# Performance work log

Measured on AMD Instinct MI355X. Metric: run time of the kernel, lower is better.

Reference implementation:

```python
import jax, jax.numpy as jnp
import numpy as np

D_MODEL = 1024
NUM_HEADS = 16
D_HEAD = D_MODEL // NUM_HEADS
NEG_BIG = 10000000000.0  # matches the torch module's -1e10 mask constant


def setup_inputs() -> dict:
    key = jax.random.key(0)
    ks = jax.random.split(key, 9)
    d = D_MODEL
    scale = 1.0 / np.sqrt(d)
    inp = {
        "x": jax.random.normal(ks[0], (2, 2048, d), dtype=jnp.float32),
        "W_q": jax.random.normal(ks[1], (d, d), dtype=jnp.float32) * scale,
        "b_q": jnp.zeros((d,), dtype=jnp.float32),
        "W_k": jax.random.normal(ks[2], (d, d), dtype=jnp.float32) * scale,
        "b_k": jnp.zeros((d,), dtype=jnp.float32),
        "W_v": jax.random.normal(ks[3], (d, d), dtype=jnp.float32) * scale,
        "b_v": jnp.zeros((d,), dtype=jnp.float32),
        "W_o": jax.random.normal(ks[4], (d, d), dtype=jnp.float32) * scale,
        "b_o": jnp.zeros((d,), dtype=jnp.float32),
    }
    return inp


def reference(x, W_q, b_q, W_k, b_k, W_v, b_v, W_o, b_o):
    B, S, d = x.shape
    H, Dh = NUM_HEADS, D_HEAD

    Q = x @ W_q + b_q  # [B,S,d]
    K = x @ W_k + b_k
    V = x @ W_v + b_v

    # split heads: [B,S,d] -> [B,H,S,Dh]
    Qh = Q.reshape(B, S, H, Dh).transpose(0, 2, 1, 3)
    Kh = K.reshape(B, S, H, Dh).transpose(0, 2, 1, 3)
    Vh = V.reshape(B, S, H, Dh).transpose(0, 2, 1, 3)

    scores = jnp.einsum("bhid,bhjd->bhij", Qh, Kh) / jnp.sqrt(
        jnp.asarray(Dh, dtype=x.dtype)
    )

    # causal mask: tril(scores) - 1e10 * (1 - tril_mask)
    causal = jnp.tril(jnp.ones((S, S), dtype=x.dtype))
    scores = scores * causal - NEG_BIG * (1.0 - causal)

    attn = jax.nn.softmax(scores, axis=-1)  # dropout p=0.0 -> identity

    vals = jnp.einsum("bhij,bhjd->bhid", attn, Vh)  # [B,H,S,Dh]
    vals = vals.transpose(0, 2, 1, 3).reshape(B, S, d)

    return vals @ W_o + b_o
```

## Files before the change

### kernel.cpp

```cpp
#include <hip/hip_runtime.h>

typedef unsigned short u16;
typedef __attribute__((ext_vector_type(8))) short short8;
typedef __attribute__((ext_vector_type(4))) short shortx4;
typedef __attribute__((ext_vector_type(4))) float floatx4;

#define S_ 2048
#define D_ 1024
#define DQKV_ 3072
#define H_ 16
#define DH_ 64

#define EXP2F(x) __builtin_amdgcn_exp2f(x)

template <bool B> struct BoolC { static constexpr bool value = B; };

__device__ __forceinline__ float bf2f(u16 x) {
    union { unsigned int u; float f; } v; v.u = ((unsigned int)x) << 16; return v.f;
}
__device__ __forceinline__ u16 f2bf(float f) {
    unsigned int u = __float_as_uint(f);
    return (u16)((u + 0x7fffu + ((u >> 16) & 1u)) >> 16);
}
__device__ __forceinline__ unsigned int cvtpk_bf16(float lo, float hi) {
    unsigned int r;
    asm("v_cvt_pk_bf16_f32 %0, %1, %2" : "=v"(r) : "v"(lo), "v"(hi));
    return r;
}

__device__ __forceinline__ void async16(const void* g, void* l) {
    __builtin_amdgcn_global_load_lds(
        (const __attribute__((address_space(1))) unsigned int*)g,
        (__attribute__((address_space(3))) unsigned int*)l, 16, 0, 0);
}

__global__ __launch_bounds__(256) void convert_x(const float* __restrict__ x, u16* __restrict__ xb) {
    const size_t i = ((size_t)blockIdx.x * 256 + threadIdx.x) * 4;
    float4 v = *(const float4*)&x[i];
    shortx4 h;
    h[0] = (short)f2bf(v.x); h[1] = (short)f2bf(v.y);
    h[2] = (short)f2bf(v.z); h[3] = (short)f2bf(v.w);
    *(shortx4*)&xb[i] = h;
}

__global__ __launch_bounds__(256) void transpose_w4(const float* __restrict__ Wq, const float* __restrict__ Wk,
                                                    const float* __restrict__ Wv, const float* __restrict__ Wo,
                                                    u16* __restrict__ Wqkvt, u16* __restrict__ Wot) {
    __shared__ u16 tile[32][33];
    const int z = blockIdx.z;
    const float* W = (z == 0) ? Wq : (z == 1) ? Wk : (z == 2) ? Wv : Wo;
    u16* dst = (z == 3) ? Wot : (Wqkvt + (size_t)z * D_ * D_);
    const int tx = threadIdx.x, ty = threadIdx.y;
    const int n0 = blockIdx.x * 32, k0 = blockIdx.y * 32;
#pragma unroll
    for (int r = 0; r < 4; ++r) {
        int k = ty + r * 8;
        tile[k][tx] = f2bf(W[(size_t)(k0 + k) * D_ + n0 + tx]);
    }
    __syncthreads();
#pragma unroll
    for (int r = 0; r < 4; ++r) {
        int n = ty + r * 8;
        dst[(size_t)(n0 + n) * D_ + k0 + tx] = tile[tx][n];
    }
}

__global__ __launch_bounds__(256) void transpose_headV(const u16* __restrict__ QKV, u16* __restrict__ Vt) {
    __shared__ u16 tile[64 * 65];
    const int t = threadIdx.x;
    const int bh = blockIdx.y, b = bh >> 4, h = bh & 15;
    const int s0 = blockIdx.x << 6;
#pragma unroll
    for (int i = 0; i < 16; ++i) {
        int idx = t + (i << 8);
        int s = idx >> 6, d = idx & 63;
        tile[s * 65 + d] = QKV[(size_t)(b * S_ + s0 + s) * DQKV_ + 2048 + h * DH_ + d];
    }
    __syncthreads();
#pragma unroll
    for (int i = 0; i < 16; ++i) {
        int idx = t + (i << 8);
        int d = idx >> 6, p = idx & 63;
        int sk = ((p >> 5) << 5) | (((p >> 2) & 1) << 4) | (((p >> 3) & 3) << 2) | (p & 3);
        Vt[((size_t)bh * DH_ + d) * S_ + s0 + p] = tile[sk * 65 + d];
    }
}

template <int BM, int BN, bool OUTF32>
__global__ __launch_bounds__(256) void gemm_bt(const u16* __restrict__ A, const u16* __restrict__ Bt,
                                               const float* __restrict__ b0, const float* __restrict__ b1,
                                               const float* __restrict__ b2, void* __restrict__ Cp,
                                               int M, int N, int Kd) {
    constexpr int FI = BM / 32, FJ = BN / 32;
    __shared__ __align__(16) u16 As[2][BM * 32];
    __shared__ __align__(16) u16 Bs[2][BN * 32];
    const int t = threadIdx.x;
    const int m0 = blockIdx.y * BM, n0 = blockIdx.x * BN;
    const int w = t >> 6, lane = t & 63;
    const int lr = lane & 15, lg = lane >> 4;
    const int wm = (w >> 1) * (BM / 2), wn = (w & 1) * (BN / 2);
    const int srow = lane >> 2, scol = (lane & 3) << 3;
    floatx4 acc[FI][FJ] = {};

    auto stage = [&](int buf, int k0) {
#pragma unroll
        for (int c = 0; c < BM / 64; ++c) {
            int rbase = (w * (BM / 64) + c) * 16;
            async16(&A[(size_t)(m0 + rbase + srow) * Kd + k0 + scol], &As[buf][rbase * 32]);
        }
#pragma unroll
        for (int c = 0; c < BN / 64; ++c) {
            int rbase = (w * (BN / 64) + c) * 16;
            async16(&Bt[(size_t)(n0 + rbase + srow) * Kd + k0 + scol], &Bs[buf][rbase * 32]);
        }
    };

    stage(0, 0);
    const int nk = Kd / 32;
    for (int kk = 0; kk < nk; ++kk) {
        const int cur = kk & 1;
        __syncthreads();
        if (kk + 1 < nk) stage(cur ^ 1, (kk + 1) * 32);

        short8 af[FI], bfr[FJ];
#pragma unroll
        for (int i = 0; i < FI; ++i) af[i]  = *(const short8*)&As[cur][(wm + i * 16 + lr) * 32 + lg * 8];
#pragma unroll
        for (int j = 0; j < FJ; ++j) bfr[j] = *(const short8*)&Bs[cur][(wn + j * 16 + lr) * 32 + lg * 8];
#pragma unroll
        for (int i = 0; i < FI; ++i)
#pragma unroll
            for (int j = 0; j < FJ; ++j)
                acc[i][j] = __builtin_amdgcn_mfma_f32_16x16x32_bf16(af[i], bfr[j], acc[i][j], 0, 0, 0);
    }

#pragma unroll
    for (int j = 0; j < FJ; ++j) {
        int col = n0 + wn + j * 16 + lr;
        const float* bp = (col < 1024) ? b0 : (col < 2048) ? b1 : b2;
        float bv = bp[col & 1023];
#pragma unroll
        for (int i = 0; i < FI; ++i) {
            int rb = m0 + wm + i * 16 + lg * 4;
#pragma unroll
            for (int ii = 0; ii < 4; ++ii) {
                float val = acc[i][j][ii] + bv;
                if (OUTF32) ((float*)Cp)[(size_t)(rb + ii) * N + col] = val;
                else        ((u16*)Cp)[(size_t)(rb + ii) * N + col] = f2bf(val);
            }
        }
    }
}

__global__ __launch_bounds__(256) void attn_mfma(const u16* __restrict__ QKV, const u16* __restrict__ Vt,
                                                 u16* __restrict__ O) {
    __shared__ __align__(16) u16 KsA[2][64 * 64];
    __shared__ __align__(16) u16 VsA[2][64 * 64];
    const int t = threadIdx.x, w = t >> 6, lane = t & 63;
    const int lr = lane & 15, lg = lane >> 4;
    const int bh = blockIdx.x, b = bh >> 4, h = bh & 15;
    const int qt = 31 - blockIdx.y;
    const int q0 = qt << 6;
    const float cs = 0.18033688f;

    const u16* Kb  = QKV + (size_t)b * S_ * DQKV_ + 1024 + h * DH_;
    const u16* Vtb = Vt + (size_t)bh * DH_ * S_;

    const int rb = lane >> 3;
    const int cc = ((lane & 7) ^ rb) << 3;
    const int swz = lr & 7;

    short8 qf[2];
#pragma unroll
    for (int ks = 0; ks < 2; ++ks)
        qf[ks] = *(const short8*)&QKV[(size_t)(b * S_ + q0 + w * 16 + lr) * DQKV_ + h * DH_ + ks * 32 + lg * 8];

    floatx4 of[4] = {};
    float lsum = 0.f;

    auto stage = [&](int buf, int kbase) {
        u16* Kd = &KsA[buf][w * 512];
        u16* Vd = &VsA[buf][w * 512];
        async16(&Kb[(size_t)(kbase + w * 8 + rb) * DQKV_ + cc], Kd);
        async16(&Kb[(size_t)(kbase + 32 + w * 8 + rb) * DQKV_ + cc], Kd + 2048);
        async16(&Vtb[(size_t)(w * 8 + rb) * S_ + kbase + cc], Vd);
        async16(&Vtb[(size_t)(32 + w * 8 + rb) * S_ + kbase + cc], Vd + 2048);
    };

    stage(0, 0);

    auto body = [&](int kb, auto diagc) {
        constexpr bool DIAG = decltype(diagc)::value;
        const int cur = kb & 1;
        __syncthreads();
        if (kb < qt) stage(cur ^ 1, (kb + 1) << 6);
        const u16* Kc = KsA[cur];
        const u16* Vc = VsA[cur];

        floatx4 sf[4] = {};
#pragma unroll
        for (int ks = 0; ks < 2; ++ks)
#pragma unroll
            for (int tt = 0; tt < 4; ++tt) {
                short8 kf = *(const short8*)&Kc[(tt * 16 + lr) * 64 + ((((ks << 2) + lg) ^ swz) << 3)];
                sf[tt] = __builtin_amdgcn_mfma_f32_16x16x32_bf16(kf, qf[ks], sf[tt], 0, 0, 0);
            }

        float ev[4][4];
#pragma unroll
        for (int tt = 0; tt < 4; ++tt) {
            float s0;
#pragma unroll
            for (int ii = 0; ii < 4; ++ii) {
                float e = EXP2F(sf[tt][ii] * cs);
                if (DIAG && (tt * 16 + lg * 4 + ii > w * 16 + lr)) e = 0.f;
                ev[tt][ii] = e;
                s0 = (ii == 0) ? e : s0 + e;
            }
            lsum += s0;
        }

#pragma unroll
        for (int ks = 0; ks < 2; ++ks) {
            union { short8 s; unsigned int u[4]; } pk;
            pk.u[0] = cvtpk_bf16(ev[2 * ks][0], ev[2 * ks][1]);
            pk.u[1] = cvtpk_bf16(ev[2 * ks][2], ev[2 * ks][3]);
            pk.u[2] = cvtpk_bf16(ev[2 * ks + 1][0], ev[2 * ks + 1][1]);
            pk.u[3] = cvtpk_bf16(ev[2 * ks + 1][2], ev[2 * ks + 1][3]);
#pragma unroll
            for (int tt = 0; tt < 4; ++tt) {
                short8 vf = *(const short8*)&Vc[(tt * 16 + lr) * 64 + ((((ks << 2) + lg) ^ swz) << 3)];
                of[tt] = __builtin_amdgcn_mfma_f32_16x16x32_bf16(pk.s, vf, of[tt], 0, 0, 0);
            }
        }
    };

    for (int kb = 0; kb < qt; ++kb) body(kb, BoolC<false>{});
    body(qt, BoolC<true>{});

    lsum += __shfl_xor(lsum, 16);
    lsum += __shfl_xor(lsum, 32);
    const float rinv = 1.f / lsum;
    float rv[4];
#pragma unroll
    for (int ii = 0; ii < 4; ++ii)
        rv[ii] = __shfl(rinv, (lane & 48) | (lg * 4 + ii));

#pragma unroll
    for (int tt = 0; tt < 4; ++tt)
#pragma unroll
        for (int ii = 0; ii < 4; ++ii)
            O[(size_t)(b * S_ + q0 + w * 16 + lg * 4 + ii) * D_ + h * DH_ + tt * 16 + lr] =
                f2bf(of[tt][ii] * rv[ii]);
}

extern "C" void kernel_launch(void* const* d_in, const int* in_sizes, int n_in,
                              void* d_out, int out_size, void* d_ws, size_t ws_size,
                              hipStream_t stream) {
    (void)in_sizes; (void)n_in; (void)out_size; (void)ws_size;
    const float* x  = (const float*)d_in[0];
    const float* Wq = (const float*)d_in[1];
    const float* bq = (const float*)d_in[2];
    const float* Wk = (const float*)d_in[3];
    const float* bk = (const float*)d_in[4];
    const float* Wv = (const float*)d_in[5];
    const float* bv = (const float*)d_in[6];
    const float* Wo = (const float*)d_in[7];
    const float* bo = (const float*)d_in[8];

    u16* ws    = (u16*)d_ws;
    u16* WqkvT = ws;
    u16* WoT   = ws + (size_t)3 * (1 << 20);
    u16* QKV   = ws + (size_t)4 * (1 << 20);
    u16* Vtm   = ws + (size_t)16 * (1 << 20);
    u16* xbf   = ws + (size_t)20 * (1 << 20);
    u16* Am    = ws + (size_t)20 * (1 << 20);

    convert_x<<<4096, 256, 0, stream>>>(x, xbf);
    transpose_w4<<<dim3(32, 32, 4), dim3(32, 8), 0, stream>>>(Wq, Wk, Wv, Wo, WqkvT, WoT);

    gemm_bt<128, 128, false><<<dim3(DQKV_ / 128, 4096 / 128), 256, 0, stream>>>(
        xbf, WqkvT, bq, bk, bv, QKV, 4096, DQKV_, 1024);

    transpose_headV<<<dim3(32, 32), 256, 0, stream>>>(QKV, Vtm);

    attn_mfma<<<dim3(32, 32), 256, 0, stream>>>(QKV, Vtm, Am);

    gemm_bt<64, 128, true><<<dim3(1024 / 128, 4096 / 64), 256, 0, stream>>>(
        Am, WoT, bo, bo, bo, d_out, 4096, 1024, 1024);
}
```

Baseline: 191.1 us.

## Swizzle GEMM block order, stage bf16 epilogue through LDS, add MFMA priority hints

The GEMM remaps workgroup IDs so consecutive blocks spread across XCD-sized groups, improving L2 locality. For bf16 output it writes results into a swizzled shared-memory tile and then stores 16-byte rows coalesced, replacing scattered 2-byte stores. The attention kernel raises wave priority around its MFMA sections with s_setprio. These add extra barriers and LDS traffic in the epilogue, and the workgroup remap could hurt locality if the grid shape doesn't suit it.

```diff
diff --git a/kernel.cpp b/kernel.cpp
--- a/kernel.cpp
+++ b/kernel.cpp
@@ -92,10 +92,15 @@
                                                const float* __restrict__ b2, void* __restrict__ Cp,
                                                int M, int N, int Kd) {
     constexpr int FI = BM / 32, FJ = BN / 32;
-    __shared__ __align__(16) u16 As[2][BM * 32];
-    __shared__ __align__(16) u16 Bs[2][BN * 32];
+    __shared__ __align__(16) u16 smem[2][(BM + BN) * 32];
     const int t = threadIdx.x;
-    const int m0 = blockIdx.y * BM, n0 = blockIdx.x * BN;
+
+    const int nwg = gridDim.x * gridDim.y;
+    int fid = blockIdx.y * gridDim.x + blockIdx.x;
+    if ((nwg & 7) == 0) fid = (fid & 7) * (nwg >> 3) + (fid >> 3);
+    const int bx = fid % gridDim.x, by = fid / gridDim.x;
+    const int m0 = by * BM, n0 = bx * BN;
+
     const int w = t >> 6, lane = t & 63;
     const int lr = lane & 15, lg = lane >> 4;
     const int wm = (w >> 1) * (BM / 2), wn = (w & 1) * (BN / 2);
@@ -103,15 +108,17 @@
     floatx4 acc[FI][FJ] = {};
 
     auto stage = [&](int buf, int k0) {
+        u16* As = &smem[buf][0];
+        u16* Bs = &smem[buf][BM * 32];
 #pragma unroll
         for (int c = 0; c < BM / 64; ++c) {
             int rbase = (w * (BM / 64) + c) * 16;
-            async16(&A[(size_t)(m0 + rbase + srow) * Kd + k0 + scol], &As[buf][rbase * 32]);
+            async16(&A[(size_t)(m0 + rbase + srow) * Kd + k0 + scol], &As[rbase * 32]);
         }
 #pragma unroll
         for (int c = 0; c < BN / 64; ++c) {
             int rbase = (w * (BN / 64) + c) * 16;
-            async16(&Bt[(size_t)(n0 + rbase + srow) * Kd + k0 + scol], &Bs[buf][rbase * 32]);
+            async16(&Bt[(size_t)(n0 + rbase + srow) * Kd + k0 + scol], &Bs[rbase * 32]);
         }
     };
 
@@ -121,12 +128,14 @@
         const int cur = kk & 1;
         __syncthreads();
         if (kk + 1 < nk) stage(cur ^ 1, (kk + 1) * 32);
+        const u16* As = &smem[cur][0];
+        const u16* Bs = &smem[cur][BM * 32];
 
         short8 af[FI], bfr[FJ];
 #pragma unroll
-        for (int i = 0; i < FI; ++i) af[i]  = *(const short8*)&As[cur][(wm + i * 16 + lr) * 32 + lg * 8];
-#pragma unroll
-        for (int j = 0; j < FJ; ++j) bfr[j] = *(const short8*)&Bs[cur][(wn + j * 16 + lr) * 32 + lg * 8];
+        for (int i = 0; i < FI; ++i) af[i]  = *(const short8*)&As[(wm + i * 16 + lr) * 32 + lg * 8];
+#pragma unroll
+        for (int j = 0; j < FJ; ++j) bfr[j] = *(const short8*)&Bs[(wn + j * 16 + lr) * 32 + lg * 8];
 #pragma unroll
         for (int i = 0; i < FI; ++i)
 #pragma unroll
@@ -134,19 +143,45 @@
                 acc[i][j] = __builtin_amdgcn_mfma_f32_16x16x32_bf16(af[i], bfr[j], acc[i][j], 0, 0, 0);
     }
 
-#pragma unroll
-    for (int j = 0; j < FJ; ++j) {
-        int col = n0 + wn + j * 16 + lr;
-        const float* bp = (col < 1024) ? b0 : (col < 2048) ? b1 : b2;
-        float bv = bp[col & 1023];
-#pragma unroll
-        for (int i = 0; i < FI; ++i) {
-            int rb = m0 + wm + i * 16 + lg * 4;
-#pragma unroll
-            for (int ii = 0; ii < 4; ++ii) {
-                float val = acc[i][j][ii] + bv;
-                if (OUTF32) ((float*)Cp)[(size_t)(rb + ii) * N + col] = val;
-                else        ((u16*)Cp)[(size_t)(rb + ii) * N + col] = f2bf(val);
+    if (!OUTF32) {
+        __syncthreads();
+        u16* Cs = &smem[0][0];
+#pragma unroll
+        for (int j = 0; j < FJ; ++j) {
+            int c = wn + j * 16 + lr;
+            int col = n0 + c;
+            const float* bp = (col < 1024) ? b0 : (col < 2048) ? b1 : b2;
+            float bv = bp[col & 1023];
+#pragma unroll
+            for (int i = 0; i < FI; ++i)
+#pragma unroll
+                for (int ii = 0; ii < 4; ++ii) {
+                    int r = wm + i * 16 + lg * 4 + ii;
+                    Cs[r * BN + (c ^ ((r & 15) << 3))] = f2bf(acc[i][j][ii] + bv);
+                }
+        }
+        __syncthreads();
+        constexpr int CPR = BN / 8;
+        constexpr int ITER = BM * CPR / 256;
+#pragma unroll
+        for (int it = 0; it < ITER; ++it) {
+            int g = it * 256 + t;
+            int r = g / CPR, cc = g % CPR;
+            short8 vv = *(const short8*)&Cs[r * BN + ((cc * 8) ^ ((r & 15) << 3))];
+            *(short8*)((u16*)Cp + (size_t)(m0 + r) * N + n0 + cc * 8) = vv;
+        }
+    } else {
+#pragma unroll
+        for (int j = 0; j < FJ; ++j) {
+            int col = n0 + wn + j * 16 + lr;
+            const float* bp = (col < 1024) ? b0 : (col < 2048) ? b1 : b2;
+            float bv = bp[col & 1023];
+#pragma unroll
+            for (int i = 0; i < FI; ++i) {
+                int rb = m0 + wm + i * 16 + lg * 4;
+#pragma unroll
+                for (int ii = 0; ii < 4; ++ii)
+                    ((float*)Cp)[(size_t)(rb + ii) * N + col] = acc[i][j][ii] + bv;
             }
         }
     }
@@ -198,6 +233,7 @@
         const u16* Vc = VsA[cur];
 
         floatx4 sf[4] = {};
+        __builtin_amdgcn_s_setprio(1);
 #pragma unroll
         for (int ks = 0; ks < 2; ++ks)
 #pragma unroll
@@ -205,6 +241,7 @@
                 short8 kf = *(const short8*)&Kc[(tt * 16 + lr) * 64 + ((((ks << 2) + lg) ^ swz) << 3)];
                 sf[tt] = __builtin_amdgcn_mfma_f32_16x16x32_bf16(kf, qf[ks], sf[tt], 0, 0, 0);
             }
+        __builtin_amdgcn_s_setprio(0);
 
         float ev[4][4];
 #pragma unroll
@@ -220,6 +257,7 @@
             lsum += s0;
         }
 
+        __builtin_amdgcn_s_setprio(1);
 #pragma unroll
         for (int ks = 0; ks < 2; ++ks) {
             union { short8 s; unsigned int u[4]; } pk;
@@ -233,6 +271,7 @@
                 of[tt] = __builtin_amdgcn_mfma_f32_16x16x32_bf16(pk.s, vf, of[tt], 0, 0, 0);
             }
         }
+        __builtin_amdgcn_s_setprio(0);
     };
 
     for (int kb = 0; kb < qt; ++kb) body(kb, BoolC<false>{});
```

Result: faster. 179.4 us (-6.1%).
